# Kernel optimization log

Measured on AMD Instinct MI355X. Metric: run time of the kernel, lower is better.

## Reference

```python
import jax, jax.numpy as jnp
import numpy as np
import math

B = 16
IMG = 224
P = 16
C_IN = 3
E = 768
H = 12
HD = E // H          # 64
D = 6                # depth
MLP = 3072
NC = 1000
GH = IMG // P        # 14
N = GH * GH + 1      # 197 tokens incl cls
LAMBDA_INIT = 0.8
EPS = 1e-5


def setup_inputs() -> dict:
    key = jax.random.key(0)
    ks = jax.random.split(key, 24)
    s = 0.02
    inp = {
        "x": jax.random.normal(ks[0], (B, C_IN, IMG, IMG), jnp.float32),
        "conv_w": jax.random.normal(ks[1], (E, C_IN, P, P), jnp.float32) * s,
        "conv_b": jnp.zeros((E,), jnp.float32),
        "cls_token": jax.random.normal(ks[2], (1, 1, E), jnp.float32) * s,
        "pos_embed": jax.random.normal(ks[3], (1, N, E), jnp.float32) * s,
        # per-layer stacked params (leading dim D)
        "Wq": jax.random.normal(ks[4], (D, E, 2 * E), jnp.float32) * s,
        "Wk": jax.random.normal(ks[5], (D, E, 2 * E), jnp.float32) * s,
        "Wv": jax.random.normal(ks[6], (D, E, 2 * E), jnp.float32) * s,
        "lq1": jax.random.normal(ks[7], (D, H, HD), jnp.float32) * 0.1,
        "lk1": jax.random.normal(ks[8], (D, H, HD), jnp.float32) * 0.1,
        "lq2": jax.random.normal(ks[9], (D, H, HD), jnp.float32) * 0.1,
        "lk2": jax.random.normal(ks[10], (D, H, HD), jnp.float32) * 0.1,
        "gn_g": jnp.ones((D, 2 * HD), jnp.float32),
        "gn_b": jnp.zeros((D, 2 * HD), jnp.float32),
        "Wo": jax.random.normal(ks[11], (D, 2 * E, E), jnp.float32) * s,
        "ln1_g": jnp.ones((D, E), jnp.float32),
        "ln1_b": jnp.zeros((D, E), jnp.float32),
        "ln2_g": jnp.ones((D, E), jnp.float32),
        "ln2_b": jnp.zeros((D, E), jnp.float32),
        "mlp_w1": jax.random.normal(ks[12], (D, E, MLP), jnp.float32) * s,
        "mlp_b1": jnp.zeros((D, MLP), jnp.float32),
        "mlp_w2": jax.random.normal(ks[13], (D, MLP, E), jnp.float32) * s,
        "mlp_b2": jnp.zeros((D, E), jnp.float32),
        "lnf_g": jnp.ones((E,), jnp.float32),
        "lnf_b": jnp.zeros((E,), jnp.float32),
        "head_w": jax.random.normal(ks[14], (E, NC), jnp.float32) * s,
        "head_b": jnp.zeros((NC,), jnp.float32),
    }
    return inp


def _ln(z, g, b):
    m = jnp.mean(z, axis=-1, keepdims=True)
    v = jnp.var(z, axis=-1, keepdims=True)
    return (z - m) * jax.lax.rsqrt(v + EPS) * g + b


def _forward(x, conv_w, conv_b, cls_token, pos_embed, Wq, Wk, Wv,
             lq1, lk1, lq2, lk2, gn_g, gn_b, Wo,
             ln1_g, ln1_b, ln2_g, ln2_b,
             mlp_w1, mlp_b1, mlp_w2, mlp_b2,
             lnf_g, lnf_b, head_w, head_b):
    Bx = x.shape[0]
    # patch embedding (conv stride=kernel == non-overlapping patch matmul)
    xp = x.reshape(Bx, C_IN, GH, P, GH, P)
    tok = jnp.einsum('bchpwq,ecpq->bhwe', xp, conv_w).reshape(Bx, GH * GH, E) + conv_b
    h = jnp.concatenate([jnp.broadcast_to(cls_token, (Bx, 1, E)), tok], axis=1) + pos_embed

    scale = 1.0 / math.sqrt(HD)

    def block(h, p):
        xn = _ln(h, p['ln1_g'], p['ln1_b'])
        q = (xn @ p['Wq']).reshape(Bx, N, H, 2 * HD).transpose(0, 2, 1, 3)
        k = (xn @ p['Wk']).reshape(Bx, N, H, 2 * HD).transpose(0, 2, 1, 3)
        v = (xn @ p['Wv']).reshape(Bx, N, H, 2 * HD).transpose(0, 2, 1, 3)
        q1, q2 = q[..., :HD], q[..., HD:]
        k1, k2 = k[..., :HD], k[..., HD:]
        a1 = jax.nn.softmax(jnp.einsum('bhnd,bhmd->bhnm', q1, k1) * scale, axis=-1)
        a2 = jax.nn.softmax(jnp.einsum('bhnd,bhmd->bhnm', q2, k2) * scale, axis=-1)
        lam = (jnp.exp(jnp.sum(p['lq1'] * p['lk1'], axis=-1))
               - jnp.exp(jnp.sum(p['lq2'] * p['lk2'], axis=-1)) + LAMBDA_INIT)  # (H,)
        attn = a1 - lam[None, :, None, None] * a2
        o = jnp.einsum('bhnm,bhmd->bhnd', attn, v)  # (B,H,N,2HD)
        # GroupNorm(1 group) over (N, 2HD) per (b,h) sample, per-channel affine
        m = jnp.mean(o, axis=(2, 3), keepdims=True)
        var = jnp.var(o, axis=(2, 3), keepdims=True)
        o = (o - m) * jax.lax.rsqrt(var + EPS) * p['gn_g'] + p['gn_b']
        o = o.transpose(0, 2, 1, 3).reshape(Bx, N, 2 * E) @ p['Wo']
        h = h + o
        xn2 = _ln(h, p['ln2_g'], p['ln2_b'])
        ff = jax.nn.gelu(xn2 @ p['mlp_w1'] + p['mlp_b1'], approximate=False) @ p['mlp_w2'] + p['mlp_b2']
        return h + ff, attn

    params = dict(Wq=Wq, Wk=Wk, Wv=Wv, lq1=lq1, lk1=lk1, lq2=lq2, lk2=lk2,
                  gn_g=gn_g, gn_b=gn_b, Wo=Wo, ln1_g=ln1_g, ln1_b=ln1_b,
                  ln2_g=ln2_g, ln2_b=ln2_b, mlp_w1=mlp_w1, mlp_b1=mlp_b1,
                  mlp_w2=mlp_w2, mlp_b2=mlp_b2)
    h, attns = jax.lax.scan(block, h, params)
    h = _ln(h, lnf_g, lnf_b)
    logits = h[:, 0] @ head_w + head_b
    return logits, attns  # attns: (D, B, H, N, N)


def reference(x, conv_w, conv_b, cls_token, pos_embed, Wq, Wk, Wv,
              lq1, lk1, lq2, lk2, gn_g, gn_b, Wo,
              ln1_g, ln1_b, ln2_g, ln2_b,
              mlp_w1, mlp_b1, mlp_w2, mlp_b2,
              lnf_g, lnf_b, head_w, head_b):
    return _forward(x, conv_w, conv_b, cls_token, pos_embed, Wq, Wk, Wv,
                    lq1, lk1, lq2, lk2, gn_g, gn_b, Wo,
                    ln1_g, ln1_b, ln2_g, ln2_b,
                    mlp_w1, mlp_b1, mlp_w2, mlp_b2,
                    lnf_g, lnf_b, head_w, head_b)
```

## Files before the change

### kernel.cpp

```cpp
#include <hip/hip_runtime.h>
#include <hip/hip_bf16.h>
#include <math.h>

#define BB 16
#define NT 197
#define EE 768
#define HH 12
#define E2 1536
#define MLPD 3072
#define NCLS 1000
#define ND 6
#define EPSF 1e-5f
#define SCALEF 0.125f
#define LAMINIT 0.8f
#define TOKC 3152

using v8bf  = __attribute__((ext_vector_type(8))) __bf16;
using f32x4 = __attribute__((ext_vector_type(4))) float;
typedef __hip_bfloat16 bf16;

#define AS1 __attribute__((address_space(1)))
#define AS3 __attribute__((address_space(3)))

__device__ __forceinline__ void gld16(const void* g, void* l) {
    __builtin_amdgcn_global_load_lds((const AS1 void*)g, (AS3 void*)l, 16, 0, 0);
}

__device__ __forceinline__ float gelu_f(float x) {
    const float u = x + 0.044715f * x * x * x;
    const float e = __expf(fminf(1.5957691216f * u, 80.f));
    return x * e / (e + 1.f);
}

__global__ __launch_bounds__(256) void gemm_bf16(
    const bf16* __restrict__ A, const bf16* __restrict__ Wt,
    const float* __restrict__ bias, float* __restrict__ C0,
    float* __restrict__ C1, float* __restrict__ C2,
    const float* __restrict__ pos, int M, int K, int ldA, int ldB, int Nc, int mode)
{
    __shared__ __align__(16) unsigned char smem[32768];
    const int t = threadIdx.x;
    const int wave = t >> 6, lane = t & 63;
    const int wr = wave >> 1, wc = wave & 1;
    const int lr = lane & 15, lk = lane >> 4;

    const int bid0 = blockIdx.y * gridDim.x + blockIdx.x;
    const int nwg = gridDim.x * gridDim.y;
    const int qv = nwg >> 3, rv = nwg & 7;
    const int xcd = bid0 & 7, ii = bid0 >> 3;
    const int wgid = (xcd < rv ? xcd * (qv + 1) : rv * (qv + 1) + (xcd - rv) * qv) + ii;
    const int rowBase = (wgid / gridDim.x) * 128;
    const int colBase = (wgid % gridDim.x) * 128;
    const size_t zoff = (size_t)blockIdx.z * K * 2;

    f32x4 acc[4][4];
#pragma unroll
    for (int i = 0; i < 4; ++i)
#pragma unroll
        for (int j = 0; j < 4; ++j) acc[i][j] = (f32x4){0.f,0.f,0.f,0.f};

    const size_t ldA2 = (size_t)ldA * 2, ldB2 = (size_t)ldB * 2;
    const int srow = t >> 3;
    const int schunk = (t & 7) ^ ((t >> 3) & 7);
    const char* Abase = (const char*)A + zoff + schunk * 16;
    const char* Bbase = (const char*)Wt + zoff + schunk * 16;
    unsigned char* lA = smem + t * 16;
    unsigned char* lB = smem + 16384 + t * 16;
    const v8bf* Sa = (const v8bf*)smem;
    const v8bf* Sb = (const v8bf*)(smem + 16384);

    int rA[4], rB[4];
#pragma unroll
    for (int c = 0; c < 4; ++c) {
        rA[c] = min(rowBase + c * 32 + srow, M - 1);
        rB[c] = colBase + c * 32 + srow;
    }

    for (int k0 = 0; k0 < K; k0 += 64) {
        const size_t kb = (size_t)k0 * 2;
#pragma unroll
        for (int c = 0; c < 4; ++c) {
            gld16(Abase + (size_t)rA[c] * ldA2 + kb, lA + c * 4096);
            gld16(Bbase + (size_t)rB[c] * ldB2 + kb, lB + c * 4096);
        }
        __syncthreads();
#pragma unroll
        for (int s = 0; s < 2; ++s) {
            const int xr_ = (s * 4 + lk) ^ (lr & 7);
            v8bf af[4], bfr[4];
#pragma unroll
            for (int i = 0; i < 4; ++i) af[i] = Sa[(wr * 64 + i * 16 + lr) * 8 + xr_];
#pragma unroll
            for (int j = 0; j < 4; ++j) bfr[j] = Sb[(wc * 64 + j * 16 + lr) * 8 + xr_];
#pragma unroll
            for (int i = 0; i < 4; ++i)
#pragma unroll
                for (int j = 0; j < 4; ++j)
                    acc[i][j] = __builtin_amdgcn_mfma_f32_16x16x32_bf16(af[i], bfr[j], acc[i][j], 0, 0, 0);
        }
        __syncthreads();
    }

    if (mode == 0) {
        float* Cs = (float*)smem;
        float* C0z = C0 + (size_t)blockIdx.z * M * Nc;
#pragma unroll
        for (int half = 0; half < 2; ++half) {
            __syncthreads();
            if (wr == half) {
#pragma unroll
                for (int i = 0; i < 4; ++i)
#pragma unroll
                    for (int j = 0; j < 4; ++j)
#pragma unroll
                        for (int rr = 0; rr < 4; ++rr)
                            Cs[(i*16 + lk*4 + rr)*128 + wc*64 + j*16 + lr] = acc[i][j][rr];
            }
            __syncthreads();
#pragma unroll
            for (int k = 0; k < 8; ++k) {
                const int idx = k*256 + t;
                const int row = idx >> 5, c4 = idx & 31;
                const int r = rowBase + half*64 + row;
                if (r < M)
                    *(float4*)&C0z[(size_t)r*Nc + colBase + c4*4] = *(float4*)&Cs[row*128 + c4*4];
            }
        }
    } else if (mode == 1) {
        const int which = colBase / E2;
        if (which == 2) {
#pragma unroll
            for (int i = 0; i < 4; ++i)
#pragma unroll
                for (int j = 0; j < 4; ++j)
#pragma unroll
                    for (int rr = 0; rr < 4; ++rr) {
                        const int r = rowBase + wr * 64 + i * 16 + lk * 4 + rr;
                        const int c = colBase + wc * 64 + j * 16 + lr;
                        if (r >= M) continue;
                        const int b_ = r / NT, n_ = r % NT;
                        const int cc = c % E2;
                        const int h_ = cc >> 7, d_ = cc & 127;
                        const size_t bh = (size_t)(b_ * HH + h_);
                        ((bf16*)C2)[((bh * 7 + (n_ >> 5)) * 8 + (d_ >> 4)) * 512 +
                                    (size_t)(((d_ & 15) + (((n_ >> 3) & 3) << 4)) * 8 + (n_ & 7))] =
                            __float2bfloat16(acc[i][j][rr]);
                    }
        } else {
            const int hFix = (colBase % E2) >> 7;
            bf16* dstBase = (bf16*)(which == 0 ? C0 : C1);
            bf16* Cs = (bf16*)smem;
            __syncthreads();
#pragma unroll
            for (int i = 0; i < 4; ++i)
#pragma unroll
                for (int j = 0; j < 4; ++j)
#pragma unroll
                    for (int rr = 0; rr < 4; ++rr)
                        Cs[(wr*64 + i*16 + lk*4 + rr)*128 + wc*64 + j*16 + lr] =
                            __float2bfloat16(acc[i][j][rr]);
            __syncthreads();
#pragma unroll
            for (int k = 0; k < 8; ++k) {
                const int idx = k*256 + t;
                const int row = idx >> 4, c8 = idx & 15;
                const int r = rowBase + row;
                if (r < M) {
                    const int b_ = r / NT, n_ = r - b_ * NT;
                    const size_t bh = (size_t)(b_ * HH + hFix);
                    *(uint4*)(dstBase + (bh * 208 + n_) * 128 + c8 * 8) =
                        *(uint4*)&Cs[row*128 + c8*8];
                }
            }
        }
    } else if (mode == 3) {
        bf16* Cs = (bf16*)smem;
        __syncthreads();
#pragma unroll
        for (int i = 0; i < 4; ++i)
#pragma unroll
            for (int j = 0; j < 4; ++j)
#pragma unroll
                for (int rr = 0; rr < 4; ++rr) {
                    const int c = colBase + wc*64 + j*16 + lr;
                    float val = acc[i][j][rr] + bias[c];
                    Cs[(wr*64 + i*16 + lk*4 + rr)*128 + wc*64 + j*16 + lr] =
                        __float2bfloat16(gelu_f(val));
                }
        __syncthreads();
        bf16* C0b = (bf16*)C0;
#pragma unroll
        for (int k = 0; k < 8; ++k) {
            const int idx = k*256 + t;
            const int row = idx >> 4, c8 = idx & 15;
            const int r = rowBase + row;
            if (r < M)
                *(uint4*)(C0b + (size_t)r*Nc + colBase + c8*8) = *(uint4*)&Cs[row*128 + c8*8];
        }
    } else {
#pragma unroll
        for (int i = 0; i < 4; ++i)
#pragma unroll
            for (int j = 0; j < 4; ++j)
#pragma unroll
                for (int rr = 0; rr < 4; ++rr) {
                    const int r = rowBase + wr * 64 + i * 16 + lk * 4 + rr;
                    const int c = colBase + wc * 64 + j * 16 + lr;
                    if (r >= M) continue;
                    const int b_ = r / 196, p_ = r % 196;
                    C0[((size_t)(b_ * NT) + 1 + p_) * EE + c] =
                        acc[i][j][rr] + bias[c] + pos[(size_t)(1 + p_) * EE + c];
                }
    }
}

template<int NF>
__global__ __launch_bounds__(512, 2) void gemm256t(
    const bf16* __restrict__ A, const bf16* __restrict__ Wt,
    const float* __restrict__ bias, float* __restrict__ C0,
    float* __restrict__ C1, float* __restrict__ C2,
    int M, int K, int Nc, int mode)
{
    constexpr int NB = NF * 64;
    constexpr int BUFSZ = 32768 + NF * 8192;
    __shared__ __align__(16) unsigned char smem[2 * BUFSZ];
    const int t = threadIdx.x;
    const int wave = t >> 6, lane = t & 63;
    const int wm = wave >> 2, wn = wave & 3;
    const int lr = lane & 15, lk = lane >> 4;

    const int bid0 = blockIdx.y * gridDim.x + blockIdx.x;
    const int nwg = gridDim.x * gridDim.y;
    const int qv = nwg >> 3, rv = nwg & 7;
    const int xcd = bid0 & 7, ii = bid0 >> 3;
    const int wgid = (xcd < rv ? xcd * (qv + 1) : rv * (qv + 1) + (xcd - rv) * qv) + ii;
    const int rowBase = (wgid / gridDim.x) * 256;
    const int colBase = (wgid % gridDim.x) * NB;

    f32x4 acc[8][NF];
#pragma unroll
    for (int i = 0; i < 8; ++i)
#pragma unroll
        for (int j = 0; j < NF; ++j) acc[i][j] = (f32x4){0.f,0.f,0.f,0.f};

    const size_t ldK2 = (size_t)K * 2;
    const int srow = t >> 3;
    const int schunk = (t & 7) ^ (srow & 7);
    const char* Abase = (const char*)A + schunk * 16;
    const char* Bbase = (const char*)Wt + schunk * 16;

    int rA[4], rB[NF];
#pragma unroll
    for (int p = 0; p < 4; ++p) rA[p] = min(rowBase + p * 64 + srow, M - 1);
#pragma unroll
    for (int p = 0; p < NF; ++p) rB[p] = colBase + p * 64 + srow;

    {
        unsigned char* l0 = smem + t * 16;
#pragma unroll
        for (int p = 0; p < 4; ++p) gld16(Abase + (size_t)rA[p] * ldK2, l0 + p * 8192);
#pragma unroll
        for (int p = 0; p < NF; ++p) gld16(Bbase + (size_t)rB[p] * ldK2, l0 + 32768 + p * 8192);
#pragma unroll
        for (int p = 0; p < 4; ++p) gld16(Abase + (size_t)rA[p] * ldK2 + 128, l0 + BUFSZ + p * 8192);
#pragma unroll
        for (int p = 0; p < NF; ++p) gld16(Bbase + (size_t)rB[p] * ldK2 + 128, l0 + BUFSZ + 32768 + p * 8192);
        if constexpr (NF == 4) asm volatile("s_waitcnt vmcnt(8)" ::: "memory");
        else                   asm volatile("s_waitcnt vmcnt(7)" ::: "memory");
        asm volatile("s_barrier" ::: "memory");
    }

    const int NTt = K >> 6;
    for (int kt = 0; kt < NTt; ++kt) {
        const int buf = kt & 1;
        const v8bf* Sa = (const v8bf*)(smem + buf * BUFSZ);
        const v8bf* Sb = (const v8bf*)(smem + buf * BUFSZ + 32768);

        v8bf bfr[2][NF], af[2][4];
#pragma unroll
        for (int s = 0; s < 2; ++s) {
            const int x0 = s * 4 + lk;
#pragma unroll
            for (int j = 0; j < NF; ++j) {
                const int row = wn * (NF * 16) + j * 16 + lr;
                bfr[s][j] = Sb[row * 8 + (x0 ^ (lr & 7))];
            }
#pragma unroll
            for (int i = 0; i < 4; ++i) {
                const int row = wm * 128 + i * 16 + lr;
                af[s][i] = Sa[row * 8 + (x0 ^ (lr & 7))];
            }
        }
        __builtin_amdgcn_s_setprio(1);
#pragma unroll
        for (int s = 0; s < 2; ++s)
#pragma unroll
            for (int i = 0; i < 4; ++i)
#pragma unroll
                for (int j = 0; j < NF; ++j)
                    acc[i][j] = __builtin_amdgcn_mfma_f32_16x16x32_bf16(af[s][i], bfr[s][j], acc[i][j], 0, 0, 0);
        __builtin_amdgcn_s_setprio(0);

        v8bf af2[2][4];
#pragma unroll
        for (int s = 0; s < 2; ++s)
#pragma unroll
            for (int i = 0; i < 4; ++i) {
                const int row = wm * 128 + 64 + i * 16 + lr;
                af2[s][i] = Sa[row * 8 + ((s * 4 + lk) ^ (lr & 7))];
            }
        asm volatile("s_waitcnt lgkmcnt(0)" ::: "memory");
        asm volatile("s_barrier" ::: "memory");
        if (kt + 2 < NTt) {
            const size_t kb = (size_t)(kt + 2) * 128;
            unsigned char* ld = smem + buf * BUFSZ + t * 16;
#pragma unroll
            for (int p = 0; p < 4; ++p) gld16(Abase + (size_t)rA[p] * ldK2 + kb, ld + p * 8192);
#pragma unroll
            for (int p = 0; p < NF; ++p) gld16(Bbase + (size_t)rB[p] * ldK2 + kb, ld + 32768 + p * 8192);
            if constexpr (NF == 4) asm volatile("s_waitcnt vmcnt(8)" ::: "memory");
            else                   asm volatile("s_waitcnt vmcnt(7)" ::: "memory");
        } else {
            asm volatile("s_waitcnt vmcnt(0)" ::: "memory");
        }
        asm volatile("s_barrier" ::: "memory");
        __builtin_amdgcn_s_setprio(1);
#pragma unroll
        for (int s = 0; s < 2; ++s)
#pragma unroll
            for (int i = 0; i < 4; ++i)
#pragma unroll
                for (int j = 0; j < NF; ++j)
                    acc[4 + i][j] = __builtin_amdgcn_mfma_f32_16x16x32_bf16(af2[s][i], bfr[s][j], acc[4 + i][j], 0, 0, 0);
        __builtin_amdgcn_s_setprio(0);
    }

    if constexpr (NF == 4) {
        if (mode == 1) {
            const int which = colBase / E2;
            if (which == 2) {
#pragma unroll
                for (int i = 0; i < 8; ++i)
#pragma unroll
                    for (int j = 0; j < 4; ++j)
#pragma unroll
                        for (int rr = 0; rr < 4; ++rr) {
                            const int r = rowBase + wm * 128 + i * 16 + lk * 4 + rr;
                            if (r >= M) continue;
                            const int c = colBase + wn * 64 + j * 16 + lr;
                            const int b_ = r / NT, n_ = r % NT;
                            const int cc = c % E2;
                            const int h_ = cc >> 7, d_ = cc & 127;
                            const size_t bh = (size_t)(b_ * HH + h_);
                            ((bf16*)C2)[((bh * 7 + (n_ >> 5)) * 8 + (d_ >> 4)) * 512 +
                                        (size_t)(((d_ & 15) + (((n_ >> 3) & 3) << 4)) * 8 + (n_ & 7))] =
                                __float2bfloat16(acc[i][j][rr]);
                        }
            } else {
                bf16* dstBase = (bf16*)(which == 0 ? C0 : C1);
                const int h0 = (colBase % E2) >> 7;
                bf16* Cs = (bf16*)smem;
                __syncthreads();
#pragma unroll
                for (int i = 0; i < 8; ++i)
#pragma unroll
                    for (int j = 0; j < 4; ++j)
#pragma unroll
                        for (int rr = 0; rr < 4; ++rr)
                            Cs[(wm*128 + i*16 + lk*4 + rr)*256 + wn*64 + j*16 + lr] =
                                __float2bfloat16(acc[i][j][rr]);
                __syncthreads();
#pragma unroll
                for (int k = 0; k < 16; ++k) {
                    const int idx = k * 512 + t;
                    const int row = idx >> 5, c8 = idx & 31;
                    const int r = rowBase + row;
                    if (r < M) {
                        const int b_ = r / NT, n_ = r - b_ * NT;
                        const size_t bh = (size_t)(b_ * HH + h0 + (c8 >> 4));
                        *(uint4*)(dstBase + (bh * 208 + n_) * 128 + (size_t)(c8 & 15) * 8) =
                            *(uint4*)&Cs[row * 256 + c8 * 8];
                    }
                }
            }
            return;
        }
    }
    {
        bf16* Cs = (bf16*)smem;
        __syncthreads();
#pragma unroll
        for (int i = 0; i < 8; ++i)
#pragma unroll
            for (int j = 0; j < NF; ++j) {
                const int c = colBase + wn * (NF * 16) + j * 16 + lr;
                const float bv = bias[c];
#pragma unroll
                for (int rr = 0; rr < 4; ++rr)
                    Cs[(wm*128 + i*16 + lk*4 + rr)*NB + wn*(NF*16) + j*16 + lr] =
                        __float2bfloat16(gelu_f(acc[i][j][rr] + bv));
            }
        __syncthreads();
        bf16* C0b = (bf16*)C0;
        constexpr int CW = NB / 8;
        constexpr int ITER = 256 * CW / 512;
#pragma unroll
        for (int k = 0; k < ITER; ++k) {
            const int idx = k * 512 + t;
            const int row = idx / CW, c8 = idx - row * CW;
            const int r = rowBase + row;
            if (r < M)
                *(uint4*)(C0b + (size_t)r * Nc + colBase + c8 * 8) =
                    *(uint4*)&Cs[row * NB + c8 * 8];
        }
    }
}

__global__ __launch_bounds__(64) void attn_mfma(
    const bf16* __restrict__ Qrm, const bf16* __restrict__ Krm,
    const bf16* __restrict__ Vf, const float* __restrict__ lamp,
    float* __restrict__ aout, float* __restrict__ o, float* __restrict__ stats)
{
    const int lane = threadIdx.x;
    const int fid = blockIdx.x;
    const int xcd = fid & 7, rest = fid >> 3;
    const int qt = rest % 13, g = rest / 13;
    const int bh = g * 8 + xcd;
    const int hh = bh % HH;
    const int lr = lane & 15, lk = lane >> 4;

    __shared__ __align__(16) bf16 P[16][232];

    {
        const int r = lane & 15, c0 = 192 + (lane >> 4) * 10;
#pragma unroll
        for (int j = 0; j < 10; ++j) P[r][c0 + j] = __float2bfloat16(0.f);
    }

    v8bf qa[4];
    const bf16* Qb = Qrm + ((size_t)bh * 208 + qt * 16) * 128;
#pragma unroll
    for (int kk = 0; kk < 4; ++kk)
        qa[kk] = *(const v8bf*)(Qb + lr * 128 + kk * 32 + lk * 8);

    const bf16* Kb = Krm + (size_t)bh * 208 * 128;
    const f32x4 zf = {0.f, 0.f, 0.f, 0.f};
    f32x4 s1[13], s2[13];
#pragma unroll
    for (int t = 0; t < 13; ++t) {
        const bf16* Kt = Kb + (t * 16 + lr) * 128 + lk * 8;
        const v8bf k0 = *(const v8bf*)(Kt);
        const v8bf k1 = *(const v8bf*)(Kt + 32);
        const v8bf k2 = *(const v8bf*)(Kt + 64);
        const v8bf k3 = *(const v8bf*)(Kt + 96);
        s1[t] = __builtin_amdgcn_mfma_f32_16x16x32_bf16(qa[1], k1,
                __builtin_amdgcn_mfma_f32_16x16x32_bf16(qa[0], k0, zf, 0, 0, 0), 0, 0, 0);
        s2[t] = __builtin_amdgcn_mfma_f32_16x16x32_bf16(qa[3], k3,
                __builtin_amdgcn_mfma_f32_16x16x32_bf16(qa[2], k2, zf, 0, 0, 0), 0, 0, 0);
    }

    float m1[4] = {-1e30f,-1e30f,-1e30f,-1e30f}, m2[4] = {-1e30f,-1e30f,-1e30f,-1e30f};
#pragma unroll
    for (int t = 0; t < 13; ++t) {
        const bool kv = (t * 16 + lr) < NT;
#pragma unroll
        for (int rr = 0; rr < 4; ++rr) {
            s1[t][rr] = kv ? s1[t][rr] * SCALEF : -1e30f;
            s2[t][rr] = kv ? s2[t][rr] * SCALEF : -1e30f;
            m1[rr] = fmaxf(m1[rr], s1[t][rr]);
            m2[rr] = fmaxf(m2[rr], s2[t][rr]);
        }
    }
#pragma unroll
    for (int off = 8; off >= 1; off >>= 1)
#pragma unroll
        for (int rr = 0; rr < 4; ++rr) {
            m1[rr] = fmaxf(m1[rr], __shfl_xor(m1[rr], off));
            m2[rr] = fmaxf(m2[rr], __shfl_xor(m2[rr], off));
        }

    float z1[4] = {0,0,0,0}, z2[4] = {0,0,0,0};
#pragma unroll
    for (int t = 0; t < 13; ++t)
#pragma unroll
        for (int rr = 0; rr < 4; ++rr) {
            const float e1 = __expf(s1[t][rr] - m1[rr]);
            const float e2 = __expf(s2[t][rr] - m2[rr]);
            s1[t][rr] = e1; s2[t][rr] = e2;
            z1[rr] += e1; z2[rr] += e2;
        }
#pragma unroll
    for (int off = 8; off >= 1; off >>= 1)
#pragma unroll
        for (int rr = 0; rr < 4; ++rr) {
            z1[rr] += __shfl_xor(z1[rr], off);
            z2[rr] += __shfl_xor(z2[rr], off);
        }
    const float lam = lamp[hh];
    float r1[4], r2[4];
#pragma unroll
    for (int rr = 0; rr < 4; ++rr) { r1[rr] = 1.f / z1[rr]; r2[rr] = lam / z2[rr]; }

    __syncthreads();
#pragma unroll
    for (int t = 0; t < 13; ++t) {
        const int m_ = t * 16 + lr;
#pragma unroll
        for (int rr = 0; rr < 4; ++rr) {
            const float p = s1[t][rr] * r1[rr] - s2[t][rr] * r2[rr];
            const int n_ = lk * 4 + rr;
            P[n_][m_] = __float2bfloat16(p);
            const int n_g = qt * 16 + n_;
            if (m_ < NT && n_g < NT)
                aout[((size_t)bh * NT + n_g) * NT + m_] = p;
        }
    }
    __syncthreads();

    f32x4 oacc[8];
#pragma unroll
    for (int dt = 0; dt < 8; ++dt) oacc[dt] = zf;
    const v8bf* Vp = (const v8bf*)(Vf + (size_t)bh * 7 * 8 * 512);
    const bf16* Pb = &P[0][0];
#pragma unroll
    for (int mk = 0; mk < 7; ++mk) {
        const v8bf pa = *(const v8bf*)(Pb + lr * 232 + mk * 32 + lk * 8);
#pragma unroll
        for (int dt = 0; dt < 8; ++dt)
            oacc[dt] = __builtin_amdgcn_mfma_f32_16x16x32_bf16(
                pa, Vp[(mk * 8 + dt) * 64 + lane], oacc[dt], 0, 0, 0);
    }
#pragma unroll
    for (int dt = 0; dt < 8; ++dt)
#pragma unroll
        for (int rr = 0; rr < 4; ++rr) {
            const int n_g = qt * 16 + lk * 4 + rr;
            if (n_g < NT)
                o[((size_t)bh * NT + n_g) * 128 + dt * 16 + lr] = oacc[dt][rr];
        }

    float s = 0.f, ss = 0.f;
#pragma unroll
    for (int dt = 0; dt < 8; ++dt)
#pragma unroll
        for (int rr = 0; rr < 4; ++rr) {
            const int n_g = qt * 16 + lk * 4 + rr;
            const float vv = (n_g < NT) ? oacc[dt][rr] : 0.f;
            s += vv; ss += vv * vv;
        }
#pragma unroll
    for (int off = 32; off >= 1; off >>= 1) {
        s  += __shfl_xor(s, off);
        ss += __shfl_xor(ss, off);
    }
    if (lane == 0) {
        stats[(bh * 13 + qt) * 2]     = s;
        stats[(bh * 13 + qt) * 2 + 1] = ss;
    }
}

__global__ __launch_bounds__(256) void gn_apply(
    const float* __restrict__ o, const float* __restrict__ stats,
    const float* __restrict__ g, const float* __restrict__ bb, bf16* __restrict__ o2)
{
    const int bh = blockIdx.y, qq = blockIdx.x;
    const int t = threadIdx.x;
    float S = 0.f, SS = 0.f;
#pragma unroll
    for (int j = 0; j < 13; ++j) {
        S  += stats[(bh * 13 + j) * 2];
        SS += stats[(bh * 13 + j) * 2 + 1];
    }
    const float inv = 1.f / (float)(NT * 128);
    const float mean = S * inv;
    const float var  = SS * inv - mean * mean;
    const float rstd = rsqrtf(var + EPSF);
    const int b_ = bh / HH, h_ = bh % HH;
    const float4* ob = (const float4*)(o + (size_t)bh * NT * 128);
    const float4* g4 = (const float4*)g;
    const float4* b4 = (const float4*)bb;
    for (int idx = t; idx < 50 * 32; idx += 256) {
        const int n_ = qq * 50 + (idx >> 5);
        if (n_ >= NT) continue;
        const int d4 = idx & 31;
        const float4 v4 = ob[n_ * 32 + d4];
        const float4 gg = g4[d4], bv = b4[d4];
        bf16 tmp[4];
        tmp[0] = __float2bfloat16((v4.x - mean) * rstd * gg.x + bv.x);
        tmp[1] = __float2bfloat16((v4.y - mean) * rstd * gg.y + bv.y);
        tmp[2] = __float2bfloat16((v4.z - mean) * rstd * gg.z + bv.z);
        tmp[3] = __float2bfloat16((v4.w - mean) * rstd * gg.w + bv.w);
        *(uint2*)(o2 + ((size_t)(b_ * NT + n_)) * E2 + h_ * 128 + d4 * 4) = *(uint2*)tmp;
    }
}

__global__ __launch_bounds__(256) void ln_rows(
    const float* __restrict__ in, const float* __restrict__ g,
    const float* __restrict__ bb, bf16* __restrict__ out)
{
    const int r = blockIdx.x;
    const int t = threadIdx.x;
    const float* x = in + (size_t)r * EE;
    const float v0 = x[t], v1 = x[t+256], v2 = x[t+512];
    __shared__ float rs[256], rss[256];
    rs[t]  = v0+v1+v2;
    rss[t] = v0*v0+v1*v1+v2*v2;
    __syncthreads();
    for (int st = 128; st > 0; st >>= 1) {
        if (t < st) { rs[t] += rs[t+st]; rss[t] += rss[t+st]; }
        __syncthreads();
    }
    const float mean = rs[0] * (1.f/768.f);
    const float var  = rss[0] * (1.f/768.f) - mean*mean;
    const float rstd = rsqrtf(var + EPSF);
    bf16* o = out + (size_t)r * EE;
    o[t]     = __float2bfloat16((v0-mean)*rstd*g[t]     + bb[t]);
    o[t+256] = __float2bfloat16((v1-mean)*rstd*g[t+256] + bb[t+256]);
    o[t+512] = __float2bfloat16((v2-mean)*rstd*g[t+512] + bb[t+512]);
}

__global__ __launch_bounds__(192) void ln_fuse(
    const float* __restrict__ hin, const float* __restrict__ Pp,
    const float* __restrict__ bias, const float* __restrict__ g,
    const float* __restrict__ bb, float* __restrict__ hout, bf16* __restrict__ xout)
{
    const int r = blockIdx.x;
    const int t = threadIdx.x;
    const int lane = t & 63, wv = t >> 6;
    const size_t base4 = (size_t)r * 192 + t;
    float4 v = ((const float4*)hin)[base4];
    const float4 p0 = ((const float4*)Pp)[base4];
    const float4 p1 = ((const float4*)Pp)[(size_t)TOKC * 192 + base4];
    v.x += p0.x + p1.x; v.y += p0.y + p1.y; v.z += p0.z + p1.z; v.w += p0.w + p1.w;
    if (bias) {
        const float4 bv = ((const float4*)bias)[t];
        v.x += bv.x; v.y += bv.y; v.z += bv.z; v.w += bv.w;
    }
    float s  = v.x + v.y + v.z + v.w;
    float ss = v.x*v.x + v.y*v.y + v.z*v.z + v.w*v.w;
#pragma unroll
    for (int off = 32; off >= 1; off >>= 1) {
        s  += __shfl_xor(s, off);
        ss += __shfl_xor(ss, off);
    }
    __shared__ float ws_[3][2];
    if (lane == 0) { ws_[wv][0] = s; ws_[wv][1] = ss; }
    __syncthreads();
    const float S  = ws_[0][0] + ws_[1][0] + ws_[2][0];
    const float SS = ws_[0][1] + ws_[1][1] + ws_[2][1];
    const float mean = S * (1.f/768.f);
    const float var  = SS * (1.f/768.f) - mean*mean;
    const float rstd = rsqrtf(var + EPSF);
    ((float4*)hout)[base4] = v;
    const float4 gg = ((const float4*)g)[t];
    const float4 bv2 = ((const float4*)bb)[t];
    bf16 tmp[4];
    tmp[0] = __float2bfloat16((v.x-mean)*rstd*gg.x + bv2.x);
    tmp[1] = __float2bfloat16((v.y-mean)*rstd*gg.y + bv2.y);
    tmp[2] = __float2bfloat16((v.z-mean)*rstd*gg.z + bv2.z);
    tmp[3] = __float2bfloat16((v.w-mean)*rstd*gg.w + bv2.w);
    *(uint2*)(xout + base4 * 4) = *(uint2*)tmp;
}

__global__ void setup_misc(const float* __restrict__ conv_w, bf16* __restrict__ cwbf,
                           const float* __restrict__ cls, const float* __restrict__ pos,
                           float* __restrict__ h,
                           const float* __restrict__ lq1, const float* __restrict__ lk1,
                           const float* __restrict__ lq2, const float* __restrict__ lk2,
                           float* __restrict__ lam)
{
    const int bid = blockIdx.x;
    if (bid < 2304) {
        const int i = bid * 256 + threadIdx.x;
        cwbf[i] = __float2bfloat16(conv_w[i]);
    } else if (bid < 2352) {
        const int i = (bid - 2304) * 256 + threadIdx.x;
        const int b_ = i / EE, e_ = i % EE;
        h[(size_t)(b_*NT)*EE + e_] = cls[e_] + pos[e_];
    } else {
        const int i = threadIdx.x;
        if (i < ND*HH) {
            float d1 = 0.f, d2 = 0.f;
            for (int d = 0; d < 64; ++d) {
                d1 += lq1[i*64+d]*lk1[i*64+d];
                d2 += lq2[i*64+d]*lk2[i*64+d];
            }
            lam[i] = expf(d1) - expf(d2) + LAMINIT;
        }
    }
}

__global__ void im2col_kernel(const float* __restrict__ x, bf16* __restrict__ xcol)
{
    const int i = blockIdx.x*256 + threadIdx.x;
    if (i >= 3136*EE) return;
    const int kidx = i % EE;
    const int p_ = i / EE;
    const int b_ = p_ / 196;
    const int pp = p_ % 196;
    const int gh = pp / 14, gw = pp % 14;
    const int c_ = kidx >> 8, rr = (kidx >> 4) & 15, q_ = kidx & 15;
    xcol[i] = __float2bfloat16(x[((size_t)(b_*3 + c_)*224 + gh*16 + rr)*224 + gw*16 + q_]);
}

__global__ __launch_bounds__(256) void transpose_pack(
    const float* __restrict__ Wq, const float* __restrict__ Wk,
    const float* __restrict__ Wv, const float* __restrict__ Wo,
    const float* __restrict__ W1, const float* __restrict__ W2,
    bf16* __restrict__ wall)
{
    __shared__ float tile[2][64][65];
    int bid = blockIdx.x;
    const int dl = bid / 576; bid -= dl * 576;
    bf16* wq_t = wall + (size_t)dl * 9437184;
    bf16* wo_t = wq_t + 3538944;
    bf16* w1_t = wo_t + 1179648;
    bf16* w2_t = w1_t + 2359296;
    const float* src; bf16* dst; int K, N, gx;
    if (bid < 216) {
        const int z = bid / 72; bid -= z * 72;
        src = (z == 0 ? Wq : (z == 1 ? Wk : Wv)) + (size_t)dl * EE * E2;
        dst = wq_t + (size_t)z * E2 * EE; K = EE; N = E2; gx = 24;
    } else if (bid < 288) { src = Wo + (size_t)dl*E2*EE;  dst = wo_t; K = E2;   N = EE;   gx = 12; bid -= 216; }
    else if (bid < 432)   { src = W1 + (size_t)dl*EE*MLPD; dst = w1_t; K = EE;  N = MLPD; gx = 48; bid -= 288; }
    else                  { src = W2 + (size_t)dl*MLPD*EE; dst = w2_t; K = MLPD; N = EE;  gx = 12; bid -= 432; }
    const int bx = bid % gx, by = bid / gx;
    const int n0 = bx * 64, kbase = by * 256;
    const int t = threadIdx.x;
    const int c4 = t & 15, kr = t >> 4;
    const int ko = t & 7, nb = t >> 3;

    float4 ld[4];
#pragma unroll
    for (int i = 0; i < 4; ++i)
        ld[i] = *(const float4*)(src + (size_t)(kbase + i*16 + kr) * N + n0 + c4*4);

    for (int kt = 0; kt < 4; ++kt) {
        float (*tb)[65] = tile[kt & 1];
#pragma unroll
        for (int i = 0; i < 4; ++i) {
            const int row = i*16 + kr;
            tb[row][c4*4+0] = ld[i].x; tb[row][c4*4+1] = ld[i].y;
            tb[row][c4*4+2] = ld[i].z; tb[row][c4*4+3] = ld[i].w;
        }
        if (kt < 3) {
            const int k0n = kbase + (kt+1)*64;
#pragma unroll
            for (int i = 0; i < 4; ++i)
                ld[i] = *(const float4*)(src + (size_t)(k0n + i*16 + kr) * N + n0 + c4*4);
        }
        __syncthreads();
        const int k0 = kbase + kt*64;
#pragma unroll
        for (int i = 0; i < 2; ++i) {
            const int n = i*32 + nb;
            bf16 tmp[8];
#pragma unroll
            for (int j = 0; j < 8; ++j)
                tmp[j] = __float2bfloat16(tb[ko*8+j][n]);
            *(uint4*)(dst + (size_t)(n0 + n) * K + k0 + ko*8) = *(uint4*)tmp;
        }
    }
}

__global__ __launch_bounds__(256) void ln_cls(
    const float* __restrict__ h, const float* __restrict__ g,
    const float* __restrict__ bb, float* __restrict__ xr)
{
    const int b_ = blockIdx.x;
    const int t = threadIdx.x;
    const float* x = h + (size_t)(b_*NT)*EE;
    const float v0 = x[t], v1 = x[t+256], v2 = x[t+512];
    __shared__ float rs[256], rss[256];
    rs[t]  = v0+v1+v2;
    rss[t] = v0*v0+v1*v1+v2*v2;
    __syncthreads();
    for (int st = 128; st > 0; st >>= 1) {
        if (t < st) { rs[t] += rs[t+st]; rss[t] += rss[t+st]; }
        __syncthreads();
    }
    const float mean = rs[0] * (1.f/768.f);
    const float var  = rss[0] * (1.f/768.f) - mean*mean;
    const float rstd = rsqrtf(var + EPSF);
    float* o = xr + (size_t)b_ * EE;
    o[t]     = (v0-mean)*rstd*g[t]     + bb[t];
    o[t+256] = (v1-mean)*rstd*g[t+256] + bb[t+256];
    o[t+512] = (v2-mean)*rstd*g[t+512] + bb[t+512];
}

__global__ __launch_bounds__(256) void head_gemm(
    const float* __restrict__ xr, const float* __restrict__ hw,
    const float* __restrict__ hb, float* __restrict__ logits)
{
    const int b_ = blockIdx.y, ct = blockIdx.x;
    const int t = threadIdx.x;
    const int c_loc = t & 63, kp = t >> 6;
    const int c = ct * 64 + c_loc;
    __shared__ float xs[768];
    for (int i = t; i < 768; i += 256) xs[i] = xr[(size_t)b_*EE + i];
    __syncthreads();
    float acc = 0.f;
    if (c < NCLS) {
        const int k0 = kp * 192;
        for (int kk = k0; kk < k0 + 192; ++kk)
            acc += xs[kk] * hw[(size_t)kk * NCLS + c];
    }
    __shared__ float red[4][64];
    red[kp][c_loc] = acc;
    __syncthreads();
    if (kp == 0 && c < NCLS)
        logits[(size_t)b_*NCLS + c] =
            red[0][c_loc] + red[1][c_loc] + red[2][c_loc] + red[3][c_loc] + hb[c];
}

extern "C" void kernel_launch(void* const* d_in, const int* in_sizes, int n_in,
                              void* d_out, int out_size, void* d_ws, size_t ws_size,
                              hipStream_t stream)
{
    const float* x      = (const float*)d_in[0];
    const float* conv_w = (const float*)d_in[1];
    const float* conv_b = (const float*)d_in[2];
    const float* cls    = (const float*)d_in[3];
    const float* pos    = (const float*)d_in[4];
    const float* Wq     = (const float*)d_in[5];
    const float* Wk     = (const float*)d_in[6];
    const float* Wv     = (const float*)d_in[7];
    const float* lq1    = (const float*)d_in[8];
    const float* lk1    = (const float*)d_in[9];
    const float* lq2    = (const float*)d_in[10];
    const float* lk2    = (const float*)d_in[11];
    const float* gn_g   = (const float*)d_in[12];
    const float* gn_b   = (const float*)d_in[13];
    const float* Wo     = (const float*)d_in[14];
    const float* ln1_g  = (const float*)d_in[15];
    const float* ln1_b  = (const float*)d_in[16];
    const float* ln2_g  = (const float*)d_in[17];
    const float* ln2_b  = (const float*)d_in[18];
    const float* mlp_w1 = (const float*)d_in[19];
    const float* mlp_b1 = (const float*)d_in[20];
    const float* mlp_w2 = (const float*)d_in[21];
    const float* mlp_b2 = (const float*)d_in[22];
    const float* lnf_g  = (const float*)d_in[23];
    const float* lnf_b  = (const float*)d_in[24];
    const float* head_w = (const float*)d_in[25];
    const float* head_b = (const float*)d_in[26];

    float* out_f    = (float*)d_out;
    float* logits   = out_f;
    float* attn_out = out_f + (size_t)BB*NCLS;

    const int TOK = TOKC;
    const size_t TOKE = (size_t)TOK*EE;

    float* ws   = (float*)d_ws;
    float* h    = ws;
    float* o    = h + TOKE;
    float* Pp   = o + (size_t)BB*HH*NT*128;
    bf16*  Qrm  = (bf16*)(Pp + 2*TOKE);
    bf16*  Krm  = Qrm + (size_t)192*208*128;
    bf16*  Vf   = Krm + (size_t)192*208*128;
    bf16*  act2 = Vf + (size_t)192*7*8*512;
    bf16*  xn   = act2 + (size_t)TOK*MLPD;
    bf16*  wall = xn + TOKE;
    bf16*  cwbf = wall + (size_t)6*9437184;
    float* lam  = (float*)(cwbf + (size_t)EE*EE);
    float* xr   = lam + 128;
    float* gnst = xr + (size_t)BB*EE;

    hipMemsetAsync(Vf, 0, (size_t)192*7*8*512*2, stream);

    setup_misc<<<2353, 256, 0, stream>>>(conv_w, cwbf, cls, pos, h,
                                         lq1, lk1, lq2, lk2, lam);
    transpose_pack<<<6*576, 256, 0, stream>>>(Wq, Wk, Wv, Wo, mlp_w1, mlp_w2, wall);
    im2col_kernel<<<(3136*EE+255)/256, 256, 0, stream>>>(x, xn);
    gemm_bf16<<<dim3(EE/128, 25), 256, 0, stream>>>(
        xn, cwbf, conv_b, h, nullptr, nullptr, pos, 3136, EE, EE, EE, EE, 4);

    ln_rows<<<TOK, 256, 0, stream>>>(h, ln1_g, ln1_b, xn);

    for (int dl = 0; dl < ND; ++dl) {
        bf16* wq_t = wall + (size_t)dl*9437184;
        bf16* wo_t = wq_t + 3538944;
        bf16* w1_t = wo_t + 1179648;
        bf16* w2_t = w1_t + 2359296;

        gemm256t<4><<<dim3(4608/256, (TOK+255)/256), 512, 0, stream>>>(
            xn, wq_t, nullptr, (float*)Qrm, (float*)Krm, (float*)Vf,
            TOK, EE, 4608, 1);
        attn_mfma<<<2496, 64, 0, stream>>>(
            Qrm, Krm, Vf, lam + dl*HH, attn_out + (size_t)dl*BB*HH*NT*NT, o, gnst);
        gn_apply<<<dim3(4, BB*HH), 256, 0, stream>>>(
            o, gnst, gn_g + dl*128, gn_b + dl*128, act2);
        gemm_bf16<<<dim3(EE/128, 25, 2), 256, 0, stream>>>(
            act2, wo_t, nullptr, Pp, nullptr, nullptr, nullptr,
            TOK, E2/2, E2, E2, EE, 0);
        ln_fuse<<<TOK, 192, 0, stream>>>(
            h, Pp, nullptr, ln2_g + dl*EE, ln2_b + dl*EE, h, xn);
        gemm256t<3><<<dim3(MLPD/192, (TOK+255)/256), 512, 0, stream>>>(
            xn, w1_t, mlp_b1 + dl*MLPD, (float*)act2, nullptr, nullptr,
            TOK, EE, MLPD, 3);
        gemm_bf16<<<dim3(EE/128, 25, 2), 256, 0, stream>>>(
            act2, w2_t, nullptr, Pp, nullptr, nullptr, nullptr,
            TOK, MLPD/2, MLPD, MLPD, EE, 0);
        if (dl < ND-1)
            ln_fuse<<<TOK, 192, 0, stream>>>(
                h, Pp, mlp_b2 + dl*EE, ln1_g + (dl+1)*EE, ln1_b + (dl+1)*EE, h, xn);
        else
            ln_fuse<<<TOK, 192, 0, stream>>>(
                h, Pp, mlp_b2 + dl*EE, lnf_g, lnf_b, h, xn);
    }

    ln_cls<<<BB, 256, 0, stream>>>(h, lnf_g, lnf_b, xr);
    head_gemm<<<dim3(16, BB), 256, 0, stream>>>(xr, head_w, head_b, logits);
}
```

Before: 1.383 ms.

## Split GEMM k-tile into four LDS-load/MFMA phases with barrier interleaving

The main GEMM inner loop now handles each 64-wide k-tile in four phases (two k-halves by two row-halves) instead of loading all fragments up front. Each phase has its own LDS reads, barriers and waitcnt, and the next global prefetch is issued before the last MFMA phase. This lowers register pressure from the fragment arrays and tries to interleave LDS traffic with MFMA work across waves, at the cost of extra barriers per iteration. Separately, the weight transpose kernel drops its double-buffered tile for a single tile guarded by syncthreads, which halves its shared memory.

```diff
diff --git a/kernel.cpp b/kernel.cpp
--- a/kernel.cpp
+++ b/kernel.cpp
@@ -275,40 +275,62 @@
         const int buf = kt & 1;
         const v8bf* Sa = (const v8bf*)(smem + buf * BUFSZ);
         const v8bf* Sb = (const v8bf*)(smem + buf * BUFSZ + 32768);
-
-        v8bf bfr[2][NF], af[2][4];
-#pragma unroll
-        for (int s = 0; s < 2; ++s) {
-            const int x0 = s * 4 + lk;
-#pragma unroll
-            for (int j = 0; j < NF; ++j) {
-                const int row = wn * (NF * 16) + j * 16 + lr;
-                bfr[s][j] = Sb[row * 8 + (x0 ^ (lr & 7))];
-            }
-#pragma unroll
-            for (int i = 0; i < 4; ++i) {
-                const int row = wm * 128 + i * 16 + lr;
-                af[s][i] = Sa[row * 8 + (x0 ^ (lr & 7))];
-            }
-        }
+        v8bf af[4], bfr[NF];
+
+#pragma unroll
+        for (int j = 0; j < NF; ++j)
+            bfr[j] = Sb[(wn * (NF * 16) + j * 16 + lr) * 8 + (lk ^ (lr & 7))];
+#pragma unroll
+        for (int i = 0; i < 4; ++i)
+            af[i] = Sa[(wm * 128 + i * 16 + lr) * 8 + (lk ^ (lr & 7))];
+        asm volatile("s_barrier" ::: "memory");
+        asm volatile("s_waitcnt lgkmcnt(0)" ::: "memory");
+        __builtin_amdgcn_sched_barrier(0);
         __builtin_amdgcn_s_setprio(1);
 #pragma unroll
-        for (int s = 0; s < 2; ++s)
-#pragma unroll
-            for (int i = 0; i < 4; ++i)
-#pragma unroll
-                for (int j = 0; j < NF; ++j)
-                    acc[i][j] = __builtin_amdgcn_mfma_f32_16x16x32_bf16(af[s][i], bfr[s][j], acc[i][j], 0, 0, 0);
+        for (int i = 0; i < 4; ++i)
+#pragma unroll
+            for (int j = 0; j < NF; ++j)
+                acc[i][j] = __builtin_amdgcn_mfma_f32_16x16x32_bf16(af[i], bfr[j], acc[i][j], 0, 0, 0);
         __builtin_amdgcn_s_setprio(0);
-
-        v8bf af2[2][4];
-#pragma unroll
-        for (int s = 0; s < 2; ++s)
-#pragma unroll
-            for (int i = 0; i < 4; ++i) {
-                const int row = wm * 128 + 64 + i * 16 + lr;
-                af2[s][i] = Sa[row * 8 + ((s * 4 + lk) ^ (lr & 7))];
-            }
+        asm volatile("s_barrier" ::: "memory");
+
+#pragma unroll
+        for (int i = 0; i < 4; ++i)
+            af[i] = Sa[(wm * 128 + 64 + i * 16 + lr) * 8 + (lk ^ (lr & 7))];
+        asm volatile("s_barrier" ::: "memory");
+        asm volatile("s_waitcnt lgkmcnt(0)" ::: "memory");
+        __builtin_amdgcn_sched_barrier(0);
+        __builtin_amdgcn_s_setprio(1);
+#pragma unroll
+        for (int i = 0; i < 4; ++i)
+#pragma unroll
+            for (int j = 0; j < NF; ++j)
+                acc[4 + i][j] = __builtin_amdgcn_mfma_f32_16x16x32_bf16(af[i], bfr[j], acc[4 + i][j], 0, 0, 0);
+        __builtin_amdgcn_s_setprio(0);
+        asm volatile("s_barrier" ::: "memory");
+
+#pragma unroll
+        for (int j = 0; j < NF; ++j)
+            bfr[j] = Sb[(wn * (NF * 16) + j * 16 + lr) * 8 + ((4 + lk) ^ (lr & 7))];
+#pragma unroll
+        for (int i = 0; i < 4; ++i)
+            af[i] = Sa[(wm * 128 + i * 16 + lr) * 8 + ((4 + lk) ^ (lr & 7))];
+        asm volatile("s_barrier" ::: "memory");
+        asm volatile("s_waitcnt lgkmcnt(0)" ::: "memory");
+        __builtin_amdgcn_sched_barrier(0);
+        __builtin_amdgcn_s_setprio(1);
+#pragma unroll
+        for (int i = 0; i < 4; ++i)
+#pragma unroll
+            for (int j = 0; j < NF; ++j)
+                acc[i][j] = __builtin_amdgcn_mfma_f32_16x16x32_bf16(af[i], bfr[j], acc[i][j], 0, 0, 0);
+        __builtin_amdgcn_s_setprio(0);
+        asm volatile("s_barrier" ::: "memory");
+
+#pragma unroll
+        for (int i = 0; i < 4; ++i)
+            af[i] = Sa[(wm * 128 + 64 + i * 16 + lr) * 8 + ((4 + lk) ^ (lr & 7))];
         asm volatile("s_waitcnt lgkmcnt(0)" ::: "memory");
         asm volatile("s_barrier" ::: "memory");
         if (kt + 2 < NTt) {
@@ -318,21 +340,22 @@
             for (int p = 0; p < 4; ++p) gld16(Abase + (size_t)rA[p] * ldK2 + kb, ld + p * 8192);
 #pragma unroll
             for (int p = 0; p < NF; ++p) gld16(Bbase + (size_t)rB[p] * ldK2 + kb, ld + 32768 + p * 8192);
+        }
+        __builtin_amdgcn_sched_barrier(0);
+        __builtin_amdgcn_s_setprio(1);
+#pragma unroll
+        for (int i = 0; i < 4; ++i)
+#pragma unroll
+            for (int j = 0; j < NF; ++j)
+                acc[4 + i][j] = __builtin_amdgcn_mfma_f32_16x16x32_bf16(af[i], bfr[j], acc[4 + i][j], 0, 0, 0);
+        __builtin_amdgcn_s_setprio(0);
+        if (kt + 2 < NTt) {
             if constexpr (NF == 4) asm volatile("s_waitcnt vmcnt(8)" ::: "memory");
             else                   asm volatile("s_waitcnt vmcnt(7)" ::: "memory");
         } else {
             asm volatile("s_waitcnt vmcnt(0)" ::: "memory");
         }
         asm volatile("s_barrier" ::: "memory");
-        __builtin_amdgcn_s_setprio(1);
-#pragma unroll
-        for (int s = 0; s < 2; ++s)
-#pragma unroll
-            for (int i = 0; i < 4; ++i)
-#pragma unroll
-                for (int j = 0; j < NF; ++j)
-                    acc[4 + i][j] = __builtin_amdgcn_mfma_f32_16x16x32_bf16(af2[s][i], bfr[s][j], acc[4 + i][j], 0, 0, 0);
-        __builtin_amdgcn_s_setprio(0);
     }
 
     if constexpr (NF == 4) {
@@ -709,7 +732,7 @@
     const float* __restrict__ W1, const float* __restrict__ W2,
     bf16* __restrict__ wall)
 {
-    __shared__ float tile[2][64][65];
+    __shared__ float tile[64][65];
     int bid = blockIdx.x;
     const int dl = bid / 576; bid -= dl * 576;
     bf16* wq_t = wall + (size_t)dl * 9437184;
@@ -736,12 +759,12 @@
         ld[i] = *(const float4*)(src + (size_t)(kbase + i*16 + kr) * N + n0 + c4*4);
 
     for (int kt = 0; kt < 4; ++kt) {
-        float (*tb)[65] = tile[kt & 1];
+        if (kt) __syncthreads();
 #pragma unroll
         for (int i = 0; i < 4; ++i) {
             const int row = i*16 + kr;
-            tb[row][c4*4+0] = ld[i].x; tb[row][c4*4+1] = ld[i].y;
-            tb[row][c4*4+2] = ld[i].z; tb[row][c4*4+3] = ld[i].w;
+            tile[row][c4*4+0] = ld[i].x; tile[row][c4*4+1] = ld[i].y;
+            tile[row][c4*4+2] = ld[i].z; tile[row][c4*4+3] = ld[i].w;
         }
         if (kt < 3) {
             const int k0n = kbase + (kt+1)*64;
@@ -757,7 +780,7 @@
             bf16 tmp[8];
 #pragma unroll
             for (int j = 0; j < 8; ++j)
-                tmp[j] = __float2bfloat16(tb[ko*8+j][n]);
+                tmp[j] = __float2bfloat16(tile[ko*8+j][n]);
             *(uint4*)(dst + (size_t)(n0 + n) * K + k0 + ko*8) = *(uint4*)tmp;
         }
     }
```

After: 1.404 ms. Within noise of the previous version (+1.5%).
